# Kernel optimization log

Hardware: AMD Instinct MI355X
Metric: run time of the kernel (lower is better)

The kernel has to match this reference:

```python
import jax, jax.numpy as jnp
import numpy as np

B, T, D, H, O = 64, 512, 256, 1024, 1


def setup_inputs() -> dict:
    key = jax.random.key(0)
    ks = jax.random.split(key, 11)
    s_in = 1.0 / np.sqrt(H)
    def u(k, shape):
        return jax.random.uniform(k, shape, jnp.float32, -s_in, s_in)
    return {
        "x": jax.random.normal(ks[0], (B, T, D), jnp.float32),
        "w_ih_0": u(ks[1], (4 * H, D)),
        "w_hh_0": u(ks[2], (4 * H, H)),
        "b_ih_0": u(ks[3], (4 * H,)),
        "b_hh_0": u(ks[4], (4 * H,)),
        "w_ih_1": u(ks[5], (4 * H, H)),
        "w_hh_1": u(ks[6], (4 * H, H)),
        "b_ih_1": u(ks[7], (4 * H,)),
        "b_hh_1": u(ks[8], (4 * H,)),
        "w_lin": u(ks[9], (O, H)),
        "b_lin": u(ks[10], (O,)),
    }


def _lstm_layer(x, w_ih, w_hh, b_ih, b_hh):
    # x: [B, T, Din] -> h_seq: [B, T, H]. PyTorch gate order: i, f, g, o.
    # Precompute input projections for all timesteps (one big GEMM).
    xp = jnp.einsum("btd,gd->tbg", x, w_ih) + b_ih + b_hh  # [T, B, 4H]
    h0 = jnp.zeros((x.shape[0], w_hh.shape[1]), x.dtype)
    c0 = jnp.zeros_like(h0)

    def step(carry, xp_t):
        h, c = carry
        gates = xp_t + h @ w_hh.T  # [B, 4H]
        i, f, g, o = jnp.split(gates, 4, axis=-1)
        i = jax.nn.sigmoid(i)
        f = jax.nn.sigmoid(f)
        g = jnp.tanh(g)
        o = jax.nn.sigmoid(o)
        c = f * c + i * g
        h = o * jnp.tanh(c)
        return (h, c), h

    (_, _), h_seq = jax.lax.scan(step, (h0, c0), xp)  # h_seq: [T, B, H]
    return jnp.transpose(h_seq, (1, 0, 2))  # [B, T, H]


def reference(x, w_ih_0, w_hh_0, b_ih_0, b_hh_0,
              w_ih_1, w_hh_1, b_ih_1, b_hh_1, w_lin, b_lin):
    h1 = _lstm_layer(x, w_ih_0, w_hh_0, b_ih_0, b_hh_0)
    h2 = _lstm_layer(h1, w_ih_1, w_hh_1, b_ih_1, b_hh_1)
    return h2[:, -1, :] @ w_lin.T + b_lin  # [B, O]
```

## Files before the change

kernel.cpp:

```cpp
#include <hip/hip_runtime.h>


#define T_STEPS 512
#define NWG 256
#define LDS_W     131072
#define LDS_GBUF  (64 * 33 * 4)
#define LDS_CBUF  (64 * 9 * 4)
#define LDS_OFFS  (32 * 4)
#define SMEM_BYTES (LDS_W + LDS_GBUF + LDS_CBUF + LDS_OFFS)

typedef int v2i  __attribute__((ext_vector_type(2)));
typedef int v4i  __attribute__((ext_vector_type(4)));
typedef int v16i __attribute__((ext_vector_type(16)));

__device__ __forceinline__ v16i zero16() {
    v16i z;
#pragma unroll
    for (int i = 0; i < 16; ++i) z[i] = 0;
    return z;
}

__device__ __forceinline__ void load_f16_nw(const char* b0p, v4i* o) {
    const char* b1p = b0p + 4096;
    const char* b2p = b0p + 8192;
    const char* b3p = b0p + 12288;
    asm volatile(
        "global_load_dwordx4 %0, %16, off sc0 sc1\n\t"
        "global_load_dwordx4 %1, %16, off offset:16 sc0 sc1\n\t"
        "global_load_dwordx4 %2, %16, off offset:2048 sc0 sc1\n\t"
        "global_load_dwordx4 %3, %16, off offset:2064 sc0 sc1\n\t"
        "global_load_dwordx4 %4, %17, off sc0 sc1\n\t"
        "global_load_dwordx4 %5, %17, off offset:16 sc0 sc1\n\t"
        "global_load_dwordx4 %6, %17, off offset:2048 sc0 sc1\n\t"
        "global_load_dwordx4 %7, %17, off offset:2064 sc0 sc1\n\t"
        "global_load_dwordx4 %8, %18, off sc0 sc1\n\t"
        "global_load_dwordx4 %9, %18, off offset:16 sc0 sc1\n\t"
        "global_load_dwordx4 %10, %18, off offset:2048 sc0 sc1\n\t"
        "global_load_dwordx4 %11, %18, off offset:2064 sc0 sc1\n\t"
        "global_load_dwordx4 %12, %19, off sc0 sc1\n\t"
        "global_load_dwordx4 %13, %19, off offset:16 sc0 sc1\n\t"
        "global_load_dwordx4 %14, %19, off offset:2048 sc0 sc1\n\t"
        "global_load_dwordx4 %15, %19, off offset:2064 sc0 sc1"
        : "=&v"(o[0]), "=&v"(o[1]), "=&v"(o[2]), "=&v"(o[3]),
          "=&v"(o[4]), "=&v"(o[5]), "=&v"(o[6]), "=&v"(o[7]),
          "=&v"(o[8]), "=&v"(o[9]), "=&v"(o[10]), "=&v"(o[11]),
          "=&v"(o[12]), "=&v"(o[13]), "=&v"(o[14]), "=&v"(o[15])
        : "v"(b0p), "v"(b1p), "v"(b2p), "v"(b3p)
        : "memory");
}

#define WAIT_BIND(cntstr, b)                                                   \
    asm volatile("s_waitcnt vmcnt(" cntstr ")"                                 \
        : "+v"((b)[0]), "+v"((b)[1]), "+v"((b)[2]), "+v"((b)[3]),              \
          "+v"((b)[4]), "+v"((b)[5]), "+v"((b)[6]), "+v"((b)[7]),              \
          "+v"((b)[8]), "+v"((b)[9]), "+v"((b)[10]), "+v"((b)[11]),            \
          "+v"((b)[12]), "+v"((b)[13]), "+v"((b)[14]), "+v"((b)[15])           \
        :: "memory")

__device__ __forceinline__ void st16_wt(void* p, v4i v) {
    asm volatile("global_store_dwordx4 %0, %1, off sc0 sc1" :: "v"(p), "v"(v) : "memory");
}
__device__ __forceinline__ void store_slot(unsigned* p, unsigned v) {
    asm volatile("global_store_dword %0, %1, off sc0 sc1" :: "v"(p), "v"(v) : "memory");
}
__device__ __forceinline__ v4i ld4_mall(const unsigned* p) {
    v4i r;
    asm volatile("global_load_dwordx4 %0, %1, off sc0 sc1\n\ts_waitcnt vmcnt(0)"
                 : "=v"(r) : "v"(p) : "memory");
    return r;
}
__device__ __forceinline__ void waitcnt0() {
    asm volatile("s_waitcnt vmcnt(0)" ::: "memory");
}

__device__ __forceinline__ void split_a(v4i A0, v4i A1, v4i& HI, v4i& LO) {
    HI.x = (int)__builtin_amdgcn_perm((unsigned)A0.y, (unsigned)A0.x, 0x07050301u);
    HI.y = (int)__builtin_amdgcn_perm((unsigned)A0.w, (unsigned)A0.z, 0x07050301u);
    HI.z = (int)__builtin_amdgcn_perm((unsigned)A1.y, (unsigned)A1.x, 0x07050301u);
    HI.w = (int)__builtin_amdgcn_perm((unsigned)A1.w, (unsigned)A1.z, 0x07050301u);
    LO.x = (int)(__builtin_amdgcn_perm((unsigned)A0.y, (unsigned)A0.x, 0x06040200u) ^ 0x80808080u);
    LO.y = (int)(__builtin_amdgcn_perm((unsigned)A0.w, (unsigned)A0.z, 0x06040200u) ^ 0x80808080u);
    LO.z = (int)(__builtin_amdgcn_perm((unsigned)A1.y, (unsigned)A1.x, 0x06040200u) ^ 0x80808080u);
    LO.w = (int)(__builtin_amdgcn_perm((unsigned)A1.w, (unsigned)A1.z, 0x06040200u) ^ 0x80808080u);
}

__device__ __forceinline__ void consume8(const v4i* hb, const char* wbase,
                                         v16i& ahh, v16i& amid)
{
#pragma unroll
    for (int s = 0; s < 8; ++s) {
        v4i HI, LO; split_a(hb[2 * s], hb[2 * s + 1], HI, LO);
        v4i BH = *(const v4i*)(wbase + s * 2048);
        v4i BL = *(const v4i*)(wbase + s * 2048 + 1024);
        ahh  = __builtin_amdgcn_mfma_i32_32x32x32_i8(HI, BH, ahh, 0, 0, 0);
        amid = __builtin_amdgcn_mfma_i32_32x32x32_i8(HI, BL, amid, 0, 0, 0);
        amid = __builtin_amdgcn_mfma_i32_32x32x32_i8(LO, BH, amid, 0, 0, 0);
    }
}

__device__ __forceinline__ void kstep(const short* __restrict__ ap,
                                      const char* __restrict__ wl,
                                      v16i& ahh, v16i& amid)
{
    v4i A0 = *(const v4i*)ap;
    v4i A1 = *(const v4i*)(ap + 8);
    v4i HI, LO; split_a(A0, A1, HI, LO);
    v4i BH = *(const v4i*)wl;
    v4i BL = *(const v4i*)(wl + 1024);
    ahh  = __builtin_amdgcn_mfma_i32_32x32x32_i8(HI, BH, ahh, 0, 0, 0);
    amid = __builtin_amdgcn_mfma_i32_32x32x32_i8(HI, BL, amid, 0, 0, 0);
    amid = __builtin_amdgcn_mfma_i32_32x32x32_i8(LO, BH, amid, 0, 0, 0);
}

__global__ void quant_x(const float* __restrict__ x, short* __restrict__ xq, int n)
{
    int i = blockIdx.x * 256 + threadIdx.x;
    if (i < n) {
        float v = x[i] * 2048.f;
        v = fminf(fmaxf(v, -32767.f), 32767.f);
        xq[i] = (short)__float2int_rn(v);
    }
}

__global__ void quant_w(const float* __restrict__ wih0, const float* __restrict__ whh0,
                        const float* __restrict__ wih1, const float* __restrict__ whh1,
                        char* __restrict__ wimg)
{
    int gid = blockIdx.x * 256 + threadIdx.x;
    if (gid >= 256 * 64 * 64) return;
    int lane = gid & 63;
    int s    = (gid >> 6) & 63;
    int wg   = gid >> 12;
    int layer = wg >> 7, nblk = wg & 127;
    int col = nblk * 32 + (lane & 31);
    int ro  = (col & 3) * 1024 + (col >> 2);
    int k0  = s * 32 + (lane >> 5) * 16;
    char* dst = wimg + (size_t)wg * LDS_W + s * 2048 + lane * 16;
#pragma unroll
    for (int j = 0; j < 16; ++j) {
        int k = k0 + j;
        float w = 0.f;
        if (layer == 0) {
            if (k < 256)       w = wih0[ro * 256 + k];
            else if (k < 1280) w = whh0[ro * 1024 + (k - 256)];
        } else {
            if (k < 1024)      w = wih1[ro * 1024 + k];
            else               w = whh1[ro * 1024 + (k - 1024)];
        }
        int q  = __float2int_rn(w * 524288.f);
        int hi = (q + 128) >> 8;
        int lo = q - (hi << 8);
        dst[j]        = (char)hi;
        dst[1024 + j] = (char)lo;
    }
}

__global__ void __launch_bounds__(128) lstm_main(
    const short* __restrict__ xq, const char* __restrict__ wimg,
    const float* __restrict__ bih0, const float* __restrict__ bhh0,
    const float* __restrict__ bih1, const float* __restrict__ bhh1,
    short* __restrict__ h0q, short* __restrict__ h2q,
    float* __restrict__ h2f, unsigned* gslots)
{
    extern __shared__ char smem[];
    char*  wlds = smem;
    float* gbuf = (float*)(smem + LDS_W);
    float* cbuf = (float*)(smem + LDS_W + LDS_GBUF);
    float* offs = (float*)(smem + LDS_W + LDS_GBUF + LDS_CBUF);

    const int wg    = blockIdx.x;
    const int layer = wg >> 7;
    const int nblk  = wg & 127;
    const int tid   = threadIdx.x;
    const int lane  = tid & 63;
    const int RB    = tid >> 6;
    const float inv30 = 9.313225746154785e-10f;
    const float inv33 = 1.1641532182693481e-10f;

    {
        const v4i* src = (const v4i*)(wimg + (size_t)wg * LDS_W);
        v4i* dst = (v4i*)wlds;
        for (int i = tid; i < LDS_W / 16; i += 128) dst[i] = src[i];
    }
    for (int i = tid; i < 64 * 9; i += 128) cbuf[i] = 0.f;
    __syncthreads();

    if (tid < 32) {
        const int c  = tid;
        const int ns = (layer == 0) ? 40 : 64;
        int cs_x = 0, cs_h = 0;
        for (int s = 0; s < ns; ++s) {
            int sum = 0;
#pragma unroll
            for (int half = 0; half < 2; ++half) {
                const signed char* ph = (const signed char*)(wlds + s * 2048 + (half * 32 + c) * 16);
#pragma unroll
                for (int j = 0; j < 16; ++j)
                    sum += 256 * (int)ph[j] + (int)ph[1024 + j];
            }
            if (layer == 0 && s < 8) cs_x += sum; else cs_h += sum;
        }
        const int col = nblk * 32 + c;
        const int ro  = (col & 3) * 1024 + (col >> 2);
        const float bias = (layer == 0) ? (bih0[ro] + bhh0[ro]) : (bih1[ro] + bhh1[ro]);
        float off = 128.f * (float)cs_h * inv33 + bias;
        if (layer == 0) off += 128.f * (float)cs_x * inv30;
        offs[c] = off;
    }
    __syncthreads();

    const int mrow = RB * 32 + (lane & 31);
    const int ksub = (lane >> 5) * 16;
    const int j0   = nblk * 8;
    const int sj   = j0 >> 5;
    const int hbj  = (j0 >> 4) & 1;
    const int inj  = (j0 & 15) * 2;

    for (int p = 0; p <= T_STEPS + 1; ++p) {
        const bool actL0 = (layer == 0) && (p < T_STEPS);
        const bool actL1 = (layer == 1) && (p >= 2);
        const bool active = actL0 || actL1;

        float px[16];
        v16i ahh = zero16(), amid = zero16();

        if (actL0) {
            v16i ax = zero16(), mx = zero16();
            const short* axp = xq + ((size_t)mrow * 512 + p) * 256 + ksub;
#pragma unroll
            for (int s = 0; s < 8; ++s)
                kstep(axp + s * 32, wlds + s * 2048 + lane * 16, ax, mx);
#pragma unroll
            for (int r = 0; r < 16; ++r)
                px[r] = ((float)ax[r] * 65536.f + (float)mx[r] * 256.f) * inv30;
        } else if (actL1) {
            if (tid < 32) {
                const unsigned thr = (unsigned)(p - 1);
                const unsigned* sp = gslots + tid * 4;
                for (;;) {
                    v4i v = ld4_mall(sp);
                    bool ok = ((unsigned)v.x >= thr) && ((unsigned)v.y >= thr) &&
                              ((unsigned)v.z >= thr) && ((unsigned)v.w >= thr);
                    if (!__ballot(!ok)) break;
                    __builtin_amdgcn_s_sleep(3);
                }
            }
            __syncthreads();
            asm volatile("" ::: "memory");
            const char* f0 = (const char*)h0q + ((p - 2) & 7) * 131072
                           + RB * 65536 + lane * 32;
            v4i b0[16], b1[16];
            waitcnt0();
            const char* W = wlds + lane * 16;
            load_f16_nw(f0, b0);
            load_f16_nw(f0 + 16384, b1);
            WAIT_BIND("16", b0); consume8(b0, W, ahh, amid);
            load_f16_nw(f0 + 32768, b0);
            WAIT_BIND("16", b1); consume8(b1, W + 8 * 2048, ahh, amid);
            load_f16_nw(f0 + 49152, b1);
            WAIT_BIND("16", b0); consume8(b0, W + 16 * 2048, ahh, amid);
            WAIT_BIND("0", b1);  consume8(b1, W + 24 * 2048, ahh, amid);
        }

        if (p > 0) {
            if (tid < 64) {
                unsigned thr;
                const unsigned* sp;
                if (layer == 0) {
                    sp  = gslots + tid * 4;
                    thr = (tid < 32) ? (unsigned)p
                                     : (unsigned)(p > 5 ? p - 5 : 0);
                } else {
                    sp  = gslots + 128 + (tid & 31) * 4;
                    thr = (unsigned)p;
                }
                for (;;) {
                    v4i v = ld4_mall(sp);
                    bool ok = ((unsigned)v.x >= thr) && ((unsigned)v.y >= thr) &&
                              ((unsigned)v.z >= thr) && ((unsigned)v.w >= thr);
                    if (!__ballot(!ok)) break;
                    __builtin_amdgcn_s_sleep(3);
                }
            }
            __syncthreads();
            asm volatile("" ::: "memory");
        }

        if (active) {
            float gates[16];
            v4i b0[16], b1[16];
            if (layer == 0) {
                if (p > 0) {
                    const char* f0 = (const char*)h0q + ((p - 1) & 7) * 131072
                                   + RB * 65536 + lane * 32;
                    waitcnt0();
                    const char* W = wlds + lane * 16;
                    load_f16_nw(f0, b0);
                    load_f16_nw(f0 + 16384, b1);
                    WAIT_BIND("16", b0); consume8(b0, W + 8 * 2048, ahh, amid);
                    load_f16_nw(f0 + 32768, b0);
                    WAIT_BIND("16", b1); consume8(b1, W + 16 * 2048, ahh, amid);
                    load_f16_nw(f0 + 49152, b1);
                    WAIT_BIND("16", b0); consume8(b0, W + 24 * 2048, ahh, amid);
                    WAIT_BIND("0", b1);  consume8(b1, W + 32 * 2048, ahh, amid);
                }
#pragma unroll
                for (int r = 0; r < 16; ++r)
                    gates[r] = px[r]
                             + ((float)ahh[r] * 65536.f + (float)amid[r] * 256.f) * inv33
                             + offs[lane & 31];
            } else {
                if (p > 2) {
                    const char* f2 = (const char*)h2q + ((p - 3) & 3) * 131072
                                   + RB * 65536 + lane * 32;
                    waitcnt0();
                    const char* W = wlds + lane * 16;
                    load_f16_nw(f2, b0);
                    load_f16_nw(f2 + 16384, b1);
                    WAIT_BIND("16", b0); consume8(b0, W + 32 * 2048, ahh, amid);
                    load_f16_nw(f2 + 32768, b0);
                    WAIT_BIND("16", b1); consume8(b1, W + 40 * 2048, ahh, amid);
                    load_f16_nw(f2 + 49152, b1);
                    WAIT_BIND("16", b0); consume8(b0, W + 48 * 2048, ahh, amid);
                    WAIT_BIND("0", b1);  consume8(b1, W + 56 * 2048, ahh, amid);
                }
#pragma unroll
                for (int r = 0; r < 16; ++r)
                    gates[r] = ((float)ahh[r] * 65536.f + (float)amid[r] * 256.f) * inv33
                             + offs[lane & 31];
            }
            {
                const int rbase = RB * 32 + 4 * (lane >> 5);
                const int c = lane & 31;
#pragma unroll
                for (int r = 0; r < 16; ++r) {
                    int row = rbase + (r & 3) + 8 * (r >> 2);
                    gbuf[row * 33 + c] = gates[r];
                }
            }
        }
        __syncthreads();
        if (active && tid < 64) {
            const int r = tid;
            unsigned hq[8];
            float hf[8];
#pragma unroll
            for (int u = 0; u < 8; ++u) {
                const float gi = gbuf[r * 33 + 4 * u + 0];
                const float gf = gbuf[r * 33 + 4 * u + 1];
                const float gg = gbuf[r * 33 + 4 * u + 2];
                const float go = gbuf[r * 33 + 4 * u + 3];
                const float i_ = 1.f / (1.f + __expf(-gi));
                const float f_ = 1.f / (1.f + __expf(-gf));
                const float g_ = 1.f - 2.f / (__expf(2.f * gg) + 1.f);
                const float o_ = 1.f / (1.f + __expf(-go));
                float c_ = f_ * cbuf[r * 9 + u] + i_ * g_;
                cbuf[r * 9 + u] = c_;
                const float h_ = o_ * (1.f - 2.f / (__expf(2.f * c_) + 1.f));
                hq[u] = (unsigned)(unsigned short)(short)__float2int_rn(h_ * 16384.f);
                hf[u] = h_;
            }
            v4i pk;
            pk.x = (int)(hq[0] | (hq[1] << 16));
            pk.y = (int)(hq[2] | (hq[3] << 16));
            pk.z = (int)(hq[4] | (hq[5] << 16));
            pk.w = (int)(hq[6] | (hq[7] << 16));
            char* hw = (layer == 0)
                     ? (char*)h0q + (p & 7) * 131072
                     : (char*)h2q + ((p - 2) & 3) * 131072;
            hw += (r >> 5) * 65536 + sj * 2048 + ((r & 31) + 32 * hbj) * 32 + inj;
            st16_wt(hw, pk);
            if (layer == 1 && p == T_STEPS + 1) {
#pragma unroll
                for (int u = 0; u < 8; ++u) h2f[r * 1024 + j0 + u] = hf[u];
            }
        }
        if (p < T_STEPS + 1) {
            waitcnt0();
            __syncthreads();
            if (tid == 0)
                store_slot(gslots + wg, (unsigned)(p + 1));
        }
    }
}

__global__ void final_lin(const float* __restrict__ h2f, const float* __restrict__ wlin,
                          const float* __restrict__ blin, float* __restrict__ out)
{
    const int b = blockIdx.x;
    const int l = threadIdx.x;
    float s = 0.f;
    for (int j = l; j < 1024; j += 64) s += h2f[b * 1024 + j] * wlin[j];
#pragma unroll
    for (int off = 32; off; off >>= 1) s += __shfl_down(s, off);
    if (l == 0) out[b] = s + blin[0];
}

extern "C" void kernel_launch(void* const* d_in, const int* in_sizes, int n_in,
                              void* d_out, int out_size, void* d_ws, size_t ws_size,
                              hipStream_t stream)
{
    const float* x    = (const float*)d_in[0];
    const float* wih0 = (const float*)d_in[1];
    const float* whh0 = (const float*)d_in[2];
    const float* bih0 = (const float*)d_in[3];
    const float* bhh0 = (const float*)d_in[4];
    const float* wih1 = (const float*)d_in[5];
    const float* whh1 = (const float*)d_in[6];
    const float* bih1 = (const float*)d_in[7];
    const float* bhh1 = (const float*)d_in[8];
    const float* wlin = (const float*)d_in[9];
    const float* blin = (const float*)d_in[10];

    char* ws = (char*)d_ws;
    unsigned* gslots = (unsigned*)ws;
    short* h0q = (short*)(ws + 65536);
    short* h2q = (short*)(ws + 65536 + 1048576);
    float* h2f = (float*)(ws + 65536 + 1572864);
    short* xq  = (short*)(ws + 65536 + 1835008);
    char*  wimg = ws + 65536 + 1835008 + 16777216;

    hipMemsetAsync(ws, 0, 65536, stream);

    quant_x<<<32768, 256, 0, stream>>>(x, xq, 64 * 512 * 256);
    quant_w<<<4096, 256, 0, stream>>>(wih0, whh0, wih1, whh1, wimg);

    hipFuncSetAttribute((const void*)lstm_main,
        hipFuncAttributeMaxDynamicSharedMemorySize, SMEM_BYTES);

    lstm_main<<<NWG, 128, SMEM_BYTES, stream>>>(xq, wimg, bih0, bhh0, bih1, bhh1,
                                                h0q, h2q, h2f, gslots);
    final_lin<<<64, 64, 0, stream>>>(h2f, wlin, blin, (float*)d_out);
}
```

Before: 4.300 ms.

## Split recurrent K reduction across two wave pairs with LDS partial-sum exchange

Doubles the workgroup to 256 threads so each row block's recurrent matmul is split in half along K between two waves. Each wave handles half the h loads and MFMA work, and partial integer accumulators are merged through a new LDS exchange buffer. The x projection is folded into the integer accumulator by scaling with 8, which removes the separate float px path. This shortens the serial per-step latency of the recurrence. In exchange it adds an extra barrier and LDS traffic per step.

```diff
diff --git a/kernel.cpp b/kernel.cpp
--- a/kernel.cpp
+++ b/kernel.cpp
@@ -7,9 +7,9 @@
 #define LDS_GBUF  (64 * 33 * 4)
 #define LDS_CBUF  (64 * 9 * 4)
 #define LDS_OFFS  (32 * 4)
-#define SMEM_BYTES (LDS_W + LDS_GBUF + LDS_CBUF + LDS_OFFS)
-
-typedef int v2i  __attribute__((ext_vector_type(2)));
+#define LDS_PEX   16384
+#define SMEM_BYTES (LDS_W + LDS_GBUF + LDS_CBUF + LDS_OFFS + LDS_PEX)
+
 typedef int v4i  __attribute__((ext_vector_type(4)));
 typedef int v16i __attribute__((ext_vector_type(16)));
 
@@ -72,6 +72,10 @@
 __device__ __forceinline__ void waitcnt0() {
     asm volatile("s_waitcnt vmcnt(0)" ::: "memory");
 }
+__device__ __forceinline__ bool slots_ok(v4i v, unsigned thr) {
+    return ((unsigned)v.x >= thr) & ((unsigned)v.y >= thr) &
+           ((unsigned)v.z >= thr) & ((unsigned)v.w >= thr);
+}
 
 __device__ __forceinline__ void split_a(v4i A0, v4i A1, v4i& HI, v4i& LO) {
     HI.x = (int)__builtin_amdgcn_perm((unsigned)A0.y, (unsigned)A0.x, 0x07050301u);
@@ -155,7 +159,7 @@
     }
 }
 
-__global__ void __launch_bounds__(128) lstm_main(
+__global__ void __launch_bounds__(256, 1) lstm_main(
     const short* __restrict__ xq, const char* __restrict__ wimg,
     const float* __restrict__ bih0, const float* __restrict__ bhh0,
     const float* __restrict__ bih1, const float* __restrict__ bhh1,
@@ -167,22 +171,24 @@
     float* gbuf = (float*)(smem + LDS_W);
     float* cbuf = (float*)(smem + LDS_W + LDS_GBUF);
     float* offs = (float*)(smem + LDS_W + LDS_GBUF + LDS_CBUF);
+    int*   pexch = (int*)(smem + LDS_W + LDS_GBUF + LDS_CBUF + LDS_OFFS);
 
     const int wg    = blockIdx.x;
     const int layer = wg >> 7;
     const int nblk  = wg & 127;
     const int tid   = threadIdx.x;
     const int lane  = tid & 63;
-    const int RB    = tid >> 6;
-    const float inv30 = 9.313225746154785e-10f;
+    const int w     = tid >> 6;
+    const int RB    = w >> 1;
+    const int kh    = w & 1;
     const float inv33 = 1.1641532182693481e-10f;
 
     {
         const v4i* src = (const v4i*)(wimg + (size_t)wg * LDS_W);
         v4i* dst = (v4i*)wlds;
-        for (int i = tid; i < LDS_W / 16; i += 128) dst[i] = src[i];
-    }
-    for (int i = tid; i < 64 * 9; i += 128) cbuf[i] = 0.f;
+        for (int i = tid; i < LDS_W / 16; i += 256) dst[i] = src[i];
+    }
+    for (int i = tid; i < 64 * 9; i += 256) cbuf[i] = 0.f;
     __syncthreads();
 
     if (tid < 32) {
@@ -204,7 +210,7 @@
         const int ro  = (col & 3) * 1024 + (col >> 2);
         const float bias = (layer == 0) ? (bih0[ro] + bhh0[ro]) : (bih1[ro] + bhh1[ro]);
         float off = 128.f * (float)cs_h * inv33 + bias;
-        if (layer == 0) off += 128.f * (float)cs_x * inv30;
+        if (layer == 0) off += 128.f * (float)cs_x * 9.313225746154785e-10f;
         offs[c] = off;
     }
     __syncthreads();
@@ -221,122 +227,117 @@
         const bool actL1 = (layer == 1) && (p >= 2);
         const bool active = actL0 || actL1;
 
-        float px[16];
         v16i ahh = zero16(), amid = zero16();
 
-        if (actL0) {
+        if (layer == 0) {
             v16i ax = zero16(), mx = zero16();
-            const short* axp = xq + ((size_t)mrow * 512 + p) * 256 + ksub;
-#pragma unroll
-            for (int s = 0; s < 8; ++s)
-                kstep(axp + s * 32, wlds + s * 2048 + lane * 16, ax, mx);
-#pragma unroll
-            for (int r = 0; r < 16; ++r)
-                px[r] = ((float)ax[r] * 65536.f + (float)mx[r] * 256.f) * inv30;
-        } else if (actL1) {
-            if (tid < 32) {
-                const unsigned thr = (unsigned)(p - 1);
-                const unsigned* sp = gslots + tid * 4;
-                for (;;) {
-                    v4i v = ld4_mall(sp);
-                    bool ok = ((unsigned)v.x >= thr) && ((unsigned)v.y >= thr) &&
-                              ((unsigned)v.z >= thr) && ((unsigned)v.w >= thr);
-                    if (!__ballot(!ok)) break;
-                    __builtin_amdgcn_s_sleep(3);
+            if (actL0 && kh == 0) {
+                const short* axp = xq + ((size_t)mrow * 512 + p) * 256 + ksub;
+#pragma unroll
+                for (int s = 0; s < 8; ++s)
+                    kstep(axp + s * 32, wlds + s * 2048 + lane * 16, ax, mx);
+            }
+            if (p > 0) {
+                if (tid < 64) {
+                    const unsigned thr = (tid < 32) ? (unsigned)p
+                                                    : (unsigned)(p > 5 ? p - 5 : 0);
+                    const unsigned* sp = gslots + tid * 4;
+                    for (;;) {
+                        v4i v = ld4_mall(sp);
+                        if (!__ballot(!slots_ok(v, thr))) break;
+                        __builtin_amdgcn_s_sleep(3);
+                    }
                 }
-            }
-            __syncthreads();
-            asm volatile("" ::: "memory");
-            const char* f0 = (const char*)h0q + ((p - 2) & 7) * 131072
-                           + RB * 65536 + lane * 32;
-            v4i b0[16], b1[16];
-            waitcnt0();
-            const char* W = wlds + lane * 16;
-            load_f16_nw(f0, b0);
-            load_f16_nw(f0 + 16384, b1);
-            WAIT_BIND("16", b0); consume8(b0, W, ahh, amid);
-            load_f16_nw(f0 + 32768, b0);
-            WAIT_BIND("16", b1); consume8(b1, W + 8 * 2048, ahh, amid);
-            load_f16_nw(f0 + 49152, b1);
-            WAIT_BIND("16", b0); consume8(b0, W + 16 * 2048, ahh, amid);
-            WAIT_BIND("0", b1);  consume8(b1, W + 24 * 2048, ahh, amid);
-        }
-
-        if (p > 0) {
-            if (tid < 64) {
-                unsigned thr;
-                const unsigned* sp;
-                if (layer == 0) {
-                    sp  = gslots + tid * 4;
-                    thr = (tid < 32) ? (unsigned)p
-                                     : (unsigned)(p > 5 ? p - 5 : 0);
-                } else {
-                    sp  = gslots + 128 + (tid & 31) * 4;
-                    thr = (unsigned)p;
+                __syncthreads();
+                asm volatile("" ::: "memory");
+            }
+            if (actL0 && p > 0) {
+                const char* f0 = (const char*)h0q + ((p - 1) & 7) * 131072
+                               + RB * 65536 + lane * 32 + kh * 32768;
+                const char* W = wlds + lane * 16 + (8 + kh * 16) * 2048;
+                v4i b0[16], b1[16];
+                waitcnt0();
+                load_f16_nw(f0, b0);
+                load_f16_nw(f0 + 16384, b1);
+                WAIT_BIND("16", b0); consume8(b0, W, ahh, amid);
+                WAIT_BIND("0", b1);  consume8(b1, W + 8 * 2048, ahh, amid);
+            }
+            if (actL0 && kh == 0) {
+#pragma unroll
+                for (int r = 0; r < 16; ++r) {
+                    ahh[r]  += 8 * ax[r];
+                    amid[r] += 8 * mx[r];
                 }
-                for (;;) {
-                    v4i v = ld4_mall(sp);
-                    bool ok = ((unsigned)v.x >= thr) && ((unsigned)v.y >= thr) &&
-                              ((unsigned)v.z >= thr) && ((unsigned)v.w >= thr);
-                    if (!__ballot(!ok)) break;
-                    __builtin_amdgcn_s_sleep(3);
+            }
+        } else {
+            if (actL1) {
+                if (tid < 32) {
+                    const unsigned thr = (unsigned)(p - 1);
+                    const unsigned* sp = gslots + tid * 4;
+                    for (;;) {
+                        v4i v = ld4_mall(sp);
+                        if (!__ballot(!slots_ok(v, thr))) break;
+                        __builtin_amdgcn_s_sleep(3);
+                    }
                 }
-            }
-            __syncthreads();
-            asm volatile("" ::: "memory");
-        }
-
-        if (active) {
-            float gates[16];
-            v4i b0[16], b1[16];
-            if (layer == 0) {
-                if (p > 0) {
-                    const char* f0 = (const char*)h0q + ((p - 1) & 7) * 131072
-                                   + RB * 65536 + lane * 32;
-                    waitcnt0();
-                    const char* W = wlds + lane * 16;
-                    load_f16_nw(f0, b0);
-                    load_f16_nw(f0 + 16384, b1);
-                    WAIT_BIND("16", b0); consume8(b0, W + 8 * 2048, ahh, amid);
-                    load_f16_nw(f0 + 32768, b0);
-                    WAIT_BIND("16", b1); consume8(b1, W + 16 * 2048, ahh, amid);
-                    load_f16_nw(f0 + 49152, b1);
-                    WAIT_BIND("16", b0); consume8(b0, W + 24 * 2048, ahh, amid);
-                    WAIT_BIND("0", b1);  consume8(b1, W + 32 * 2048, ahh, amid);
+                __syncthreads();
+                asm volatile("" ::: "memory");
+                const char* f0 = (const char*)h0q + ((p - 2) & 7) * 131072
+                               + RB * 65536 + lane * 32 + kh * 32768;
+                const char* W = wlds + lane * 16 + kh * 16 * 2048;
+                v4i b0[16], b1[16];
+                waitcnt0();
+                load_f16_nw(f0, b0);
+                load_f16_nw(f0 + 16384, b1);
+                WAIT_BIND("16", b0); consume8(b0, W, ahh, amid);
+                WAIT_BIND("0", b1);  consume8(b1, W + 8 * 2048, ahh, amid);
+            }
+            if (p > 0) {
+                if (tid < 64) {
+                    const unsigned* sp = gslots + 128 + (tid & 31) * 4;
+                    const unsigned thr = (unsigned)p;
+                    for (;;) {
+                        v4i v = ld4_mall(sp);
+                        if (!__ballot(!slots_ok(v, thr))) break;
+                        __builtin_amdgcn_s_sleep(3);
+                    }
                 }
-#pragma unroll
-                for (int r = 0; r < 16; ++r)
-                    gates[r] = px[r]
-                             + ((float)ahh[r] * 65536.f + (float)amid[r] * 256.f) * inv33
-                             + offs[lane & 31];
-            } else {
-                if (p > 2) {
-                    const char* f2 = (const char*)h2q + ((p - 3) & 3) * 131072
-                                   + RB * 65536 + lane * 32;
-                    waitcnt0();
-                    const char* W = wlds + lane * 16;
-                    load_f16_nw(f2, b0);
-                    load_f16_nw(f2 + 16384, b1);
-                    WAIT_BIND("16", b0); consume8(b0, W + 32 * 2048, ahh, amid);
-                    load_f16_nw(f2 + 32768, b0);
-                    WAIT_BIND("16", b1); consume8(b1, W + 40 * 2048, ahh, amid);
-                    load_f16_nw(f2 + 49152, b1);
-                    WAIT_BIND("16", b0); consume8(b0, W + 48 * 2048, ahh, amid);
-                    WAIT_BIND("0", b1);  consume8(b1, W + 56 * 2048, ahh, amid);
-                }
-#pragma unroll
-                for (int r = 0; r < 16; ++r)
-                    gates[r] = ((float)ahh[r] * 65536.f + (float)amid[r] * 256.f) * inv33
-                             + offs[lane & 31];
-            }
-            {
-                const int rbase = RB * 32 + 4 * (lane >> 5);
-                const int c = lane & 31;
-#pragma unroll
-                for (int r = 0; r < 16; ++r) {
-                    int row = rbase + (r & 3) + 8 * (r >> 2);
-                    gbuf[row * 33 + c] = gates[r];
-                }
+                __syncthreads();
+                asm volatile("" ::: "memory");
+            }
+            if (actL1 && p > 2) {
+                const char* f2 = (const char*)h2q + ((p - 3) & 3) * 131072
+                               + RB * 65536 + lane * 32 + kh * 32768;
+                const char* W = wlds + lane * 16 + (32 + kh * 16) * 2048;
+                v4i b0[16], b1[16];
+                waitcnt0();
+                load_f16_nw(f2, b0);
+                load_f16_nw(f2 + 16384, b1);
+                WAIT_BIND("16", b0); consume8(b0, W, ahh, amid);
+                WAIT_BIND("0", b1);  consume8(b1, W + 8 * 2048, ahh, amid);
+            }
+        }
+
+        if (active && kh == 1) {
+            int* pxm = pexch + RB * 2048;
+#pragma unroll
+            for (int i = 0; i < 16; ++i) pxm[i * 64 + lane] = ahh[i];
+#pragma unroll
+            for (int i = 0; i < 16; ++i) pxm[(16 + i) * 64 + lane] = amid[i];
+        }
+        __syncthreads();
+        if (active && kh == 0) {
+            const int* pxm = pexch + RB * 2048;
+            const int rbase = RB * 32 + 4 * (lane >> 5);
+            const int c = lane & 31;
+#pragma unroll
+            for (int r = 0; r < 16; ++r) {
+                int th = ahh[r]  + pxm[r * 64 + lane];
+                int tm = amid[r] + pxm[(16 + r) * 64 + lane];
+                float g = ((float)th * 65536.f + (float)tm * 256.f) * inv33
+                        + offs[c];
+                int row = rbase + (r & 3) + 8 * (r >> 2);
+                gbuf[row * 33 + c] = g;
             }
         }
         __syncthreads();
@@ -428,7 +429,7 @@
     hipFuncSetAttribute((const void*)lstm_main,
         hipFuncAttributeMaxDynamicSharedMemorySize, SMEM_BYTES);
 
-    lstm_main<<<NWG, 128, SMEM_BYTES, stream>>>(xq, wimg, bih0, bhh0, bih1, bhh1,
+    lstm_main<<<NWG, 256, SMEM_BYTES, stream>>>(xq, wimg, bih0, bhh0, bih1, bhh1,
                                                 h0q, h2q, h2f, gslots);
     final_lin<<<64, 64, 0, stream>>>(h2f, wlin, blin, (float*)d_out);
 }
```

Measured after the change: 4.394 ms. 2.2% more time.
